# Kernel optimization log

Hardware: AMD Instinct MI355X
Metric: run time of the kernel (lower is better)

The kernel has to match this reference:

```python
import jax, jax.numpy as jnp
import numpy as np

N, C, R = 512, 32, 64   # atoms, feature channels, rbf count
EPS = 1e-8
GAMMA = 10.0
BOX = 10.0


def _eijk():
    e = np.zeros((3, 3, 3), dtype=np.float32)
    e[0, 1, 2] = e[1, 2, 0] = e[2, 0, 1] = 1.0
    e[0, 2, 1] = e[2, 1, 0] = e[1, 0, 2] = -1.0
    return jnp.asarray(e)


def setup_inputs() -> dict:
    key = jax.random.key(0)
    ks = jax.random.split(key, 8)
    d = {}
    d["geometry"] = jax.random.uniform(ks[0], (N, 3), dtype=jnp.float32) * BOX
    d["x0"] = jax.random.normal(ks[1], (N, C, 1), dtype=jnp.float32)
    d["x1"] = jax.random.normal(ks[2], (N, C, 3), dtype=jnp.float32)
    s1 = (6.0 / (R + R)) ** 0.5   # xavier_uniform for [R,R]
    s2 = (6.0 / (R + C)) ** 0.5   # xavier_uniform for [C,R]
    for i, name in enumerate(["f0", "fa", "fb", "fc"]):
        k1, k2 = jax.random.split(ks[3 + i])
        d[name + "_w1"] = jax.random.uniform(k1, (R, R), minval=-s1, maxval=s1, dtype=jnp.float32)
        d[name + "_b1"] = jnp.zeros((R,), jnp.float32)
        d[name + "_w2"] = jax.random.uniform(k2, (C, R), minval=-s2, maxval=s2, dtype=jnp.float32)
        d[name + "_b2"] = jnp.zeros((C,), jnp.float32)
    return d


def reference(geometry, x0, x1,
              f0_w1, f0_b1, f0_w2, f0_b2,
              fa_w1, fa_b1, fa_w2, fa_b2,
              fb_w1, fb_b1, fb_w2, fb_b2,
              fc_w1, fc_b1, fc_w2, fc_b2):
    # pairwise geometry: rij [N,N,3], squared dist r2 [N,N]
    rij = geometry[:, None, :] - geometry[None, :, :]
    r2 = jnp.sum(rij * rij, axis=-1)
    dij = jnp.sqrt(jnp.maximum(r2, EPS))                 # norm_with_epsilon
    centers = jnp.linspace(0.0, BOX, R, dtype=jnp.float32)
    rbf = jnp.exp(-GAMMA * (dij[..., None] - centers) ** 2)   # [N,N,R]

    self_mask = r2 < (EPS * EPS)                          # dij < EPS on true norm
    unit = rij / jnp.sqrt(r2 + EPS)[..., None]            # unit_vectors

    def radial(w1, b1, w2, b2):
        h = jax.nn.relu(jnp.einsum('abr,hr->abh', rbf, w1) + b1)
        return jnp.einsum('abh,ch->abc', h, w2) + b2      # [N,N,C]

    def f1(w1, b1, w2, b2):
        rad = jnp.where(self_mask[..., None], 0.0, radial(w1, b1, w2, b2))
        return unit[:, :, None, :] * rad[:, :, :, None]   # [N,N,C,3]

    # Filter_0 (shared radial weights) on l=0 and l=1 inputs: scalar filter, sum over neighbors b
    r0 = radial(f0_w1, f0_b1, f0_w2, f0_b2)               # [N,N,C]
    out0_a = jnp.einsum('abf,bfi->afi', r0, x0)           # [N,C,1] -> bucket 0
    out1_b = jnp.einsum('abf,bfi->afi', r0, x1)           # [N,C,3] -> bucket 1

    # filter_1_output_1 on l=0 input (cg = eye(3).unsqueeze(-1))
    F1a = f1(fa_w1, fa_b1, fa_w2, fa_b2)
    out1_a = jnp.einsum('abfi,bf->afi', F1a, x0[:, :, 0])  # [N,C,3]

    # filter_1_output_0 on l=1 input (cg = eye(3).unsqueeze(0))
    F1b = f1(fb_w1, fb_b1, fb_w2, fb_b2)
    out0_b = jnp.einsum('abfj,bfj->af', F1b, x1)[..., None]  # [N,C,1]

    # filter_1_output_1 on l=1 input (cg = eijk, cross-product coupling)
    F1c = f1(fc_w1, fc_b1, fc_w2, fc_b2)
    out1_c = jnp.einsum('ijk,abfj,bfk->afi', _eijk(), F1c, x1)  # [N,C,3]

    # concatenation() cats each bucket along channel axis (dim=-2)
    out0 = jnp.concatenate([out0_a, out0_b], axis=-2)      # [N,2C,1]
    out1 = jnp.concatenate([out1_a, out1_b, out1_c], axis=-2)  # [N,3C,3]
    return out0, out1
```

## Files before the change

### kernel.cpp

```cpp
#include <hip/hip_runtime.h>
#include <math.h>

namespace {

constexpr int NATOM = 512;
constexpr float STEP = 10.0f / 63.0f;

typedef float f32x4 __attribute__((ext_vector_type(4)));
typedef short s16x8 __attribute__((ext_vector_type(8)));

struct Ptrs { const float* p[19]; };


__device__ __forceinline__ unsigned f2bf(float f) {
  union { float f; unsigned u; } v; v.f = f;
  return (v.u + 0x7fffu + ((v.u >> 16) & 1u)) >> 16;
}

__global__ __launch_bounds__(512)
void tfn_fused(Ptrs A, float* __restrict__ out) {
  const int a    = blockIdx.x;
  const int tid  = threadIdx.x;
  const int wv   = tid >> 6;
  const int w    = wv & 3;
  const int mh   = wv >> 2;
  const int lane = tid & 63;
  const int ln   = lane & 15;
  const int hi   = lane >> 4;

  __shared__ __align__(16) short rbf_frag[2][2][2][64][8];
  __shared__ __align__(16) float u_lds[2][32][4];
  __shared__ __align__(16) short h_s[4 * 32 * 72];
  __shared__ __align__(16) float x0_s[2][32][36];
  __shared__ __align__(16) float x1_s[2][32][100];
  __shared__ __align__(16) float scr[4][16][8];

  const float* __restrict__ geom = A.p[0];
  const float* __restrict__ x0g  = A.p[1];
  const float* __restrict__ x1g  = A.p[2];

  s16x8 w1f[4][2];
  {
    const float* w1p = A.p[3 + 4 * w];
    #pragma unroll
    for (int nt = 0; nt < 4; ++nt)
      #pragma unroll
      for (int kt = 0; kt < 2; ++kt) {
        const float* src = w1p + (nt * 16 + ln) * 64 + kt * 32 + hi * 8;
        s16x8 f;
        #pragma unroll
        for (int i = 0; i < 8; ++i) f[i] = (short)f2bf(src[i]);
        w1f[nt][kt] = f;
      }
  }
  float b1v[4];
  {
    const float* b1p = A.p[4 + 4 * w];
    #pragma unroll
    for (int nt = 0; nt < 4; ++nt) b1v[nt] = b1p[nt * 16 + ln];
  }
  s16x8 w2f[2][2];
  {
    const float* w2p = A.p[5 + 4 * w];
    #pragma unroll
    for (int nt = 0; nt < 2; ++nt)
      #pragma unroll
      for (int kt = 0; kt < 2; ++kt) {
        const float* src = w2p + (nt * 16 + ln) * 64 + kt * 32 + hi * 8;
        s16x8 f;
        #pragma unroll
        for (int i = 0; i < 8; ++i) f[i] = (short)f2bf(src[i]);
        w2f[nt][kt] = f;
      }
  }
  float b2v[2];
  {
    const float* b2p = A.p[6 + 4 * w];
    b2v[0] = b2p[ln]; b2v[1] = b2p[16 + ln];
  }

  const float gax = geom[3*a+0], gay = geom[3*a+1], gaz = geom[3*a+2];

  const int sb = tid >> 4;
  const int sc = tid & 15;

  float av[8] = {0.f,0.f,0.f,0.f,0.f,0.f,0.f,0.f};

  for (int t = 0; t < 16; ++t) {
    const int b0  = t * 32;
    const int buf = t & 1;

    {
      #pragma unroll
      for (int s = 0; s < 2; ++s)
        x0_s[buf][sb][sc + 16 * s] = x0g[(b0 + sb) * 32 + sc + 16 * s];
      #pragma unroll
      for (int s = 0; s < 6; ++s)
        x1_s[buf][sb][sc + 16 * s] = x1g[(b0 + sb) * 96 + sc + 16 * s];

      const int bb = tid & 31;
      const int kq = tid >> 5;
      const int bg = b0 + bb;
      const float dx = gax - geom[3*bg+0];
      const float dy = gay - geom[3*bg+1];
      const float dz = gaz - geom[3*bg+2];
      const float r2 = dx*dx + dy*dy + dz*dz;
      const float dij = sqrtf(fmaxf(r2, 1e-8f));
      const float d0 = dij - STEP * (float)(4 * kq);
      const float d1 = d0 - STEP, d2 = d0 - 2.f*STEP, d3 = d0 - 3.f*STEP;
      const unsigned lo  = f2bf(__expf(-10.f*d0*d0)) | (f2bf(__expf(-10.f*d1*d1)) << 16);
      const unsigned hi2 = f2bf(__expf(-10.f*d2*d2)) | (f2bf(__expf(-10.f*d3*d3)) << 16);
      uint2 pk; pk.x = lo; pk.y = hi2;
      *(uint2*)&rbf_frag[buf][kq >> 3][bb >> 4][((kq >> 1) & 3) * 16 + (bb & 15)][(kq & 1) * 4] = pk;
      if (kq == 0) {
        const float inv = 1.0f / sqrtf(r2 + 1e-8f);
        f32x4 uv; uv[0] = dx*inv; uv[1] = dy*inv; uv[2] = dz*inv; uv[3] = 0.f;
        *(f32x4*)&u_lds[buf][bb][0] = uv;
      }
    }
    __syncthreads();

    const s16x8 af0 = *(const s16x8*)&rbf_frag[buf][0][mh][lane][0];
    const s16x8 af1 = *(const s16x8*)&rbf_frag[buf][1][mh][lane][0];
    f32x4 acc1[4] = {};
    #pragma unroll
    for (int nt = 0; nt < 4; ++nt)
      acc1[nt] = __builtin_amdgcn_mfma_f32_16x16x32_bf16(af0, w1f[nt][0], acc1[nt], 0, 0, 0);
    #pragma unroll
    for (int nt = 0; nt < 4; ++nt)
      acc1[nt] = __builtin_amdgcn_mfma_f32_16x16x32_bf16(af1, w1f[nt][1], acc1[nt], 0, 0, 0);
    #pragma unroll
    for (int nt = 0; nt < 4; ++nt) {
      const int j = nt * 16 + ln;
      #pragma unroll
      for (int r = 0; r < 4; ++r) {
        const int bl = mh * 16 + hi * 4 + r;
        h_s[(w * 32 + bl) * 72 + (((j >> 3) ^ (bl & 7)) << 3) + (j & 7)] =
            (short)f2bf(fmaxf(acc1[nt][r] + b1v[nt], 0.0f));
      }
    }

    const int hbase = (w * 32 + mh * 16 + ln) * 72;
    const s16x8 a20 = *(const s16x8*)&h_s[hbase + (((0 + hi) ^ (ln & 7)) << 3)];
    const s16x8 a21 = *(const s16x8*)&h_s[hbase + (((4 + hi) ^ (ln & 7)) << 3)];
    f32x4 acc2[2] = {};
    acc2[0] = __builtin_amdgcn_mfma_f32_16x16x32_bf16(a20, w2f[0][0], acc2[0], 0, 0, 0);
    acc2[1] = __builtin_amdgcn_mfma_f32_16x16x32_bf16(a20, w2f[1][0], acc2[1], 0, 0, 0);
    acc2[0] = __builtin_amdgcn_mfma_f32_16x16x32_bf16(a21, w2f[0][1], acc2[0], 0, 0, 0);
    acc2[1] = __builtin_amdgcn_mfma_f32_16x16x32_bf16(a21, w2f[1][1], acc2[1], 0, 0, 0);
    float rad0[4], rad1[4];
    #pragma unroll
    for (int e = 0; e < 4; ++e) { rad0[e] = acc2[0][e] + b2v[0]; rad1[e] = acc2[1][e] + b2v[1]; }

    const int bl4 = mh * 16 + hi * 4;
    if (w == 0) {
      #pragma unroll
      for (int e = 0; e < 4; ++e) {
        const int b = bl4 + e;
        const float r = rad0[e], s = rad1[e];
        av[0] = fmaf(r, x0_s[buf][b][ln],          av[0]);
        av[1] = fmaf(r, x1_s[buf][b][3*ln+0],      av[1]);
        av[2] = fmaf(r, x1_s[buf][b][3*ln+1],      av[2]);
        av[3] = fmaf(r, x1_s[buf][b][3*ln+2],      av[3]);
        av[4] = fmaf(s, x0_s[buf][b][16+ln],       av[4]);
        av[5] = fmaf(s, x1_s[buf][b][48+3*ln+0],   av[5]);
        av[6] = fmaf(s, x1_s[buf][b][48+3*ln+1],   av[6]);
        av[7] = fmaf(s, x1_s[buf][b][48+3*ln+2],   av[7]);
        __builtin_amdgcn_sched_barrier(0);
      }
    } else if (w == 1) {
      #pragma unroll
      for (int e = 0; e < 4; ++e) {
        const int b = bl4 + e;
        const f32x4 uv = *(const f32x4*)&u_lds[buf][b][0];
        const float rx0 = rad0[e] * x0_s[buf][b][ln];
        av[0] = fmaf(rx0, uv[0], av[0]);
        av[1] = fmaf(rx0, uv[1], av[1]);
        av[2] = fmaf(rx0, uv[2], av[2]);
        const float rx1 = rad1[e] * x0_s[buf][b][16+ln];
        av[3] = fmaf(rx1, uv[0], av[3]);
        av[4] = fmaf(rx1, uv[1], av[4]);
        av[5] = fmaf(rx1, uv[2], av[5]);
        __builtin_amdgcn_sched_barrier(0);
      }
    } else if (w == 2) {
      #pragma unroll
      for (int e = 0; e < 4; ++e) {
        const int b = bl4 + e;
        const f32x4 uv = *(const f32x4*)&u_lds[buf][b][0];
        const float dot0 = fmaf(uv[0], x1_s[buf][b][3*ln+0],
                           fmaf(uv[1], x1_s[buf][b][3*ln+1],
                                uv[2] * x1_s[buf][b][3*ln+2]));
        av[0] = fmaf(rad0[e], dot0, av[0]);
        const float dot1 = fmaf(uv[0], x1_s[buf][b][48+3*ln+0],
                           fmaf(uv[1], x1_s[buf][b][48+3*ln+1],
                                uv[2] * x1_s[buf][b][48+3*ln+2]));
        av[1] = fmaf(rad1[e], dot1, av[1]);
        __builtin_amdgcn_sched_barrier(0);
      }
    } else {
      #pragma unroll
      for (int e = 0; e < 4; ++e) {
        const int b = bl4 + e;
        const f32x4 uv = *(const f32x4*)&u_lds[buf][b][0];
        {
          const float xa = x1_s[buf][b][3*ln+0];
          const float xb = x1_s[buf][b][3*ln+1];
          const float xc = x1_s[buf][b][3*ln+2];
          const float r  = rad0[e];
          av[0] = fmaf(r, fmaf(uv[1], xc, -(uv[2] * xb)), av[0]);
          av[1] = fmaf(r, fmaf(uv[2], xa, -(uv[0] * xc)), av[1]);
          av[2] = fmaf(r, fmaf(uv[0], xb, -(uv[1] * xa)), av[2]);
        }
        {
          const float xa = x1_s[buf][b][48+3*ln+0];
          const float xb = x1_s[buf][b][48+3*ln+1];
          const float xc = x1_s[buf][b][48+3*ln+2];
          const float r  = rad1[e];
          av[3] = fmaf(r, fmaf(uv[1], xc, -(uv[2] * xb)), av[3]);
          av[4] = fmaf(r, fmaf(uv[2], xa, -(uv[0] * xc)), av[4]);
          av[5] = fmaf(r, fmaf(uv[0], xb, -(uv[1] * xa)), av[5]);
        }
        __builtin_amdgcn_sched_barrier(0);
      }
    }
  }

  #pragma unroll
  for (int q = 0; q < 8; ++q) {
    av[q] += __shfl_xor(av[q], 16);
    av[q] += __shfl_xor(av[q], 32);
  }
  if (mh == 1 && hi == 0) {
    #pragma unroll
    for (int q = 0; q < 8; ++q) scr[w][ln][q] = av[q];
  }
  __syncthreads();
  if (mh == 0 && hi == 0) {
    #pragma unroll
    for (int q = 0; q < 8; ++q) av[q] += scr[w][ln][q];
    float* o1 = out + NATOM * 64 + a * 288;
    if (w == 0) {
      out[a * 64 + ln]      = av[0];
      o1[(32 + ln) * 3 + 0] = av[1]; o1[(32 + ln) * 3 + 1] = av[2]; o1[(32 + ln) * 3 + 2] = av[3];
      out[a * 64 + 16 + ln] = av[4];
      o1[(48 + ln) * 3 + 0] = av[5]; o1[(48 + ln) * 3 + 1] = av[6]; o1[(48 + ln) * 3 + 2] = av[7];
    } else if (w == 1) {
      o1[(     ln) * 3 + 0] = av[0]; o1[(     ln) * 3 + 1] = av[1]; o1[(     ln) * 3 + 2] = av[2];
      o1[(16 + ln) * 3 + 0] = av[3]; o1[(16 + ln) * 3 + 1] = av[4]; o1[(16 + ln) * 3 + 2] = av[5];
    } else if (w == 2) {
      out[a * 64 + 32 + ln] = av[0];
      out[a * 64 + 48 + ln] = av[1];
    } else {
      o1[(64 + ln) * 3 + 0] = av[0]; o1[(64 + ln) * 3 + 1] = av[1]; o1[(64 + ln) * 3 + 2] = av[2];
      o1[(80 + ln) * 3 + 0] = av[3]; o1[(80 + ln) * 3 + 1] = av[4]; o1[(80 + ln) * 3 + 2] = av[5];
    }
  }
}

}

extern "C" void kernel_launch(void* const* d_in, const int* in_sizes, int n_in,
                              void* d_out, int out_size, void* d_ws, size_t ws_size,
                              hipStream_t stream) {
  (void)in_sizes; (void)n_in; (void)d_ws; (void)ws_size; (void)out_size;
  Ptrs A;
  for (int i = 0; i < 19; ++i) A.p[i] = (const float*)d_in[i];
  tfn_fused<<<dim3(NATOM), dim3(512), 0, stream>>>(A, (float*)d_out);
}
```

Before: 146.1 us.

## Interleave x0/x1 into one LDS array and recompute unit vectors per wave

Packs x0 and the three x1 components per channel into a single float4-aligned LDS array, so the epilogue reads two 128-bit vectors per neighbor instead of many scalar LDS loads. The unit-vector LDS buffer is dropped: waves 1-3 reload neighbor geometry from global memory and recompute the displacement and inverse norm in registers. The sched_barriers in the epilogue are removed so the compiler can reorder freely. The trade is fewer LDS loads and less LDS space against extra global geometry loads and recomputed rsqrt work per wave, plus strided global reads of x1 during staging.

```diff
diff --git a/kernel.cpp b/kernel.cpp
--- a/kernel.cpp
+++ b/kernel.cpp
@@ -29,10 +29,8 @@
   const int hi   = lane >> 4;
 
   __shared__ __align__(16) short rbf_frag[2][2][2][64][8];
-  __shared__ __align__(16) float u_lds[2][32][4];
   __shared__ __align__(16) short h_s[4 * 32 * 72];
-  __shared__ __align__(16) float x0_s[2][32][36];
-  __shared__ __align__(16) float x1_s[2][32][100];
+  __shared__ __align__(16) float xall[2][32][132];
   __shared__ __align__(16) float scr[4][16][8];
 
   const float* __restrict__ geom = A.p[0];
@@ -83,6 +81,7 @@
 
   const int sb = tid >> 4;
   const int sc = tid & 15;
+  const int bl4 = mh * 16 + hi * 4;
 
   float av[8] = {0.f,0.f,0.f,0.f,0.f,0.f,0.f,0.f};
 
@@ -90,13 +89,25 @@
     const int b0  = t * 32;
     const int buf = t & 1;
 
+    float gxe[4], gye[4], gze[4];
+    if (w != 0) {
+      const float* gp = geom + 3 * (b0 + bl4);
+      #pragma unroll
+      for (int e = 0; e < 4; ++e) {
+        gxe[e] = gp[3*e+0]; gye[e] = gp[3*e+1]; gze[e] = gp[3*e+2];
+      }
+    }
+
     {
-      #pragma unroll
-      for (int s = 0; s < 2; ++s)
-        x0_s[buf][sb][sc + 16 * s] = x0g[(b0 + sb) * 32 + sc + 16 * s];
-      #pragma unroll
-      for (int s = 0; s < 6; ++s)
-        x1_s[buf][sb][sc + 16 * s] = x1g[(b0 + sb) * 96 + sc + 16 * s];
+      const float* x0row = x0g + (b0 + sb) * 32;
+      const float* x1row = x1g + (b0 + sb) * 96;
+      f32x4 v0, v1;
+      v0[0] = x0row[sc];
+      v0[1] = x1row[3*sc+0]; v0[2] = x1row[3*sc+1]; v0[3] = x1row[3*sc+2];
+      v1[0] = x0row[sc+16];
+      v1[1] = x1row[3*(sc+16)+0]; v1[2] = x1row[3*(sc+16)+1]; v1[3] = x1row[3*(sc+16)+2];
+      *(f32x4*)&xall[buf][sb][4*sc]        = v0;
+      *(f32x4*)&xall[buf][sb][4*(sc+16)]   = v1;
 
       const int bb = tid & 31;
       const int kq = tid >> 5;
@@ -112,11 +123,6 @@
       const unsigned hi2 = f2bf(__expf(-10.f*d2*d2)) | (f2bf(__expf(-10.f*d3*d3)) << 16);
       uint2 pk; pk.x = lo; pk.y = hi2;
       *(uint2*)&rbf_frag[buf][kq >> 3][bb >> 4][((kq >> 1) & 3) * 16 + (bb & 15)][(kq & 1) * 4] = pk;
-      if (kq == 0) {
-        const float inv = 1.0f / sqrtf(r2 + 1e-8f);
-        f32x4 uv; uv[0] = dx*inv; uv[1] = dy*inv; uv[2] = dz*inv; uv[3] = 0.f;
-        *(f32x4*)&u_lds[buf][bb][0] = uv;
-      }
     }
     __syncthreads();
 
@@ -152,76 +158,50 @@
     #pragma unroll
     for (int e = 0; e < 4; ++e) { rad0[e] = acc2[0][e] + b2v[0]; rad1[e] = acc2[1][e] + b2v[1]; }
 
-    const int bl4 = mh * 16 + hi * 4;
     if (w == 0) {
       #pragma unroll
       for (int e = 0; e < 4; ++e) {
         const int b = bl4 + e;
+        const f32x4 xv0 = *(const f32x4*)&xall[buf][b][4*ln];
+        const f32x4 xv1 = *(const f32x4*)&xall[buf][b][4*(16+ln)];
         const float r = rad0[e], s = rad1[e];
-        av[0] = fmaf(r, x0_s[buf][b][ln],          av[0]);
-        av[1] = fmaf(r, x1_s[buf][b][3*ln+0],      av[1]);
-        av[2] = fmaf(r, x1_s[buf][b][3*ln+1],      av[2]);
-        av[3] = fmaf(r, x1_s[buf][b][3*ln+2],      av[3]);
-        av[4] = fmaf(s, x0_s[buf][b][16+ln],       av[4]);
-        av[5] = fmaf(s, x1_s[buf][b][48+3*ln+0],   av[5]);
-        av[6] = fmaf(s, x1_s[buf][b][48+3*ln+1],   av[6]);
-        av[7] = fmaf(s, x1_s[buf][b][48+3*ln+2],   av[7]);
-        __builtin_amdgcn_sched_barrier(0);
-      }
-    } else if (w == 1) {
+        av[0] = fmaf(r, xv0[0], av[0]);
+        av[1] = fmaf(r, xv0[1], av[1]);
+        av[2] = fmaf(r, xv0[2], av[2]);
+        av[3] = fmaf(r, xv0[3], av[3]);
+        av[4] = fmaf(s, xv1[0], av[4]);
+        av[5] = fmaf(s, xv1[1], av[5]);
+        av[6] = fmaf(s, xv1[2], av[6]);
+        av[7] = fmaf(s, xv1[3], av[7]);
+      }
+    } else {
       #pragma unroll
       for (int e = 0; e < 4; ++e) {
         const int b = bl4 + e;
-        const f32x4 uv = *(const f32x4*)&u_lds[buf][b][0];
-        const float rx0 = rad0[e] * x0_s[buf][b][ln];
-        av[0] = fmaf(rx0, uv[0], av[0]);
-        av[1] = fmaf(rx0, uv[1], av[1]);
-        av[2] = fmaf(rx0, uv[2], av[2]);
-        const float rx1 = rad1[e] * x0_s[buf][b][16+ln];
-        av[3] = fmaf(rx1, uv[0], av[3]);
-        av[4] = fmaf(rx1, uv[1], av[4]);
-        av[5] = fmaf(rx1, uv[2], av[5]);
-        __builtin_amdgcn_sched_barrier(0);
-      }
-    } else if (w == 2) {
-      #pragma unroll
-      for (int e = 0; e < 4; ++e) {
-        const int b = bl4 + e;
-        const f32x4 uv = *(const f32x4*)&u_lds[buf][b][0];
-        const float dot0 = fmaf(uv[0], x1_s[buf][b][3*ln+0],
-                           fmaf(uv[1], x1_s[buf][b][3*ln+1],
-                                uv[2] * x1_s[buf][b][3*ln+2]));
-        av[0] = fmaf(rad0[e], dot0, av[0]);
-        const float dot1 = fmaf(uv[0], x1_s[buf][b][48+3*ln+0],
-                           fmaf(uv[1], x1_s[buf][b][48+3*ln+1],
-                                uv[2] * x1_s[buf][b][48+3*ln+2]));
-        av[1] = fmaf(rad1[e], dot1, av[1]);
-        __builtin_amdgcn_sched_barrier(0);
-      }
-    } else {
-      #pragma unroll
-      for (int e = 0; e < 4; ++e) {
-        const int b = bl4 + e;
-        const f32x4 uv = *(const f32x4*)&u_lds[buf][b][0];
-        {
-          const float xa = x1_s[buf][b][3*ln+0];
-          const float xb = x1_s[buf][b][3*ln+1];
-          const float xc = x1_s[buf][b][3*ln+2];
-          const float r  = rad0[e];
-          av[0] = fmaf(r, fmaf(uv[1], xc, -(uv[2] * xb)), av[0]);
-          av[1] = fmaf(r, fmaf(uv[2], xa, -(uv[0] * xc)), av[1]);
-          av[2] = fmaf(r, fmaf(uv[0], xb, -(uv[1] * xa)), av[2]);
+        const f32x4 xv0 = *(const f32x4*)&xall[buf][b][4*ln];
+        const f32x4 xv1 = *(const f32x4*)&xall[buf][b][4*(16+ln)];
+        const float dx = gax - gxe[e], dy = gay - gye[e], dz = gaz - gze[e];
+        const float r2 = fmaf(dx, dx, fmaf(dy, dy, dz * dz));
+        const float rs = 1.0f / sqrtf(r2 + 1e-8f);
+        if (w == 1) {
+          const float t0 = rad0[e] * xv0[0] * rs;
+          av[0] = fmaf(t0, dx, av[0]); av[1] = fmaf(t0, dy, av[1]); av[2] = fmaf(t0, dz, av[2]);
+          const float t1 = rad1[e] * xv1[0] * rs;
+          av[3] = fmaf(t1, dx, av[3]); av[4] = fmaf(t1, dy, av[4]); av[5] = fmaf(t1, dz, av[5]);
+        } else if (w == 2) {
+          const float dot0 = fmaf(dx, xv0[1], fmaf(dy, xv0[2], dz * xv0[3]));
+          av[0] = fmaf(rad0[e] * rs, dot0, av[0]);
+          const float dot1 = fmaf(dx, xv1[1], fmaf(dy, xv1[2], dz * xv1[3]));
+          av[1] = fmaf(rad1[e] * rs, dot1, av[1]);
+        } else {
+          const float q0 = rad0[e] * rs, q1 = rad1[e] * rs;
+          av[0] = fmaf(q0, fmaf(dy, xv0[3], -(dz * xv0[2])), av[0]);
+          av[1] = fmaf(q0, fmaf(dz, xv0[1], -(dx * xv0[3])), av[1]);
+          av[2] = fmaf(q0, fmaf(dx, xv0[2], -(dy * xv0[1])), av[2]);
+          av[3] = fmaf(q1, fmaf(dy, xv1[3], -(dz * xv1[2])), av[3]);
+          av[4] = fmaf(q1, fmaf(dz, xv1[1], -(dx * xv1[3])), av[4]);
+          av[5] = fmaf(q1, fmaf(dx, xv1[2], -(dy * xv1[1])), av[5]);
         }
-        {
-          const float xa = x1_s[buf][b][48+3*ln+0];
-          const float xb = x1_s[buf][b][48+3*ln+1];
-          const float xc = x1_s[buf][b][48+3*ln+2];
-          const float r  = rad1[e];
-          av[3] = fmaf(r, fmaf(uv[1], xc, -(uv[2] * xb)), av[3]);
-          av[4] = fmaf(r, fmaf(uv[2], xa, -(uv[0] * xc)), av[4]);
-          av[5] = fmaf(r, fmaf(uv[0], xb, -(uv[1] * xa)), av[5]);
-        }
-        __builtin_amdgcn_sched_barrier(0);
       }
     }
   }
```

After: 177.0 us. +21.2%, slower.

## Single-buffer LDS staging, raise occupancy hint, use HIP bf16 conversion

Applied to the files above, without the earlier changes.

Replaces the double-buffered LDS staging (rbf fragments, unit vectors, x0/x1 tiles) with single buffers and adds a barrier at the top of each loop iteration to protect reuse. The smaller LDS footprint, together with a launch_bounds minimum-blocks hint of 6, is meant to let more blocks reside per CU. The hand-written float-to-bf16 rounding is swapped for the library __float2bfloat16. The cost is an extra barrier per iteration, which removes the overlap between staging the next tile and computing the current one, and the occupancy hint may force register spills.

```diff
diff --git a/kernel.cpp b/kernel.cpp
--- a/kernel.cpp
+++ b/kernel.cpp
@@ -1,4 +1,5 @@
 #include <hip/hip_runtime.h>
+#include <hip/hip_bf16.h>
 #include <math.h>
 
 namespace {
@@ -12,12 +13,13 @@
 struct Ptrs { const float* p[19]; };
 
 
-__device__ __forceinline__ unsigned f2bf(float f) {
-  union { float f; unsigned u; } v; v.f = f;
-  return (v.u + 0x7fffu + ((v.u >> 16) & 1u)) >> 16;
-}
-
-__global__ __launch_bounds__(512)
+__device__ __forceinline__ unsigned short f2bf(float f) {
+  union { __hip_bfloat16 b; unsigned short u; } v;
+  v.b = __float2bfloat16(f);
+  return v.u;
+}
+
+__global__ __launch_bounds__(512, 6)
 void tfn_fused(Ptrs A, float* __restrict__ out) {
   const int a    = blockIdx.x;
   const int tid  = threadIdx.x;
@@ -28,11 +30,11 @@
   const int ln   = lane & 15;
   const int hi   = lane >> 4;
 
-  __shared__ __align__(16) short rbf_frag[2][2][2][64][8];
-  __shared__ __align__(16) float u_lds[2][32][4];
+  __shared__ __align__(16) short rbf_frag[2][2][64][8];
   __shared__ __align__(16) short h_s[4 * 32 * 72];
-  __shared__ __align__(16) float x0_s[2][32][36];
-  __shared__ __align__(16) float x1_s[2][32][100];
+  __shared__ __align__(16) float x0_s[32][36];
+  __shared__ __align__(16) float x1_s[32][100];
+  __shared__ __align__(16) float u_lds[32][4];
   __shared__ __align__(16) float scr[4][16][8];
 
   const float* __restrict__ geom = A.p[0];
@@ -83,20 +85,22 @@
 
   const int sb = tid >> 4;
   const int sc = tid & 15;
+  const int bl4 = mh * 16 + hi * 4;
 
   float av[8] = {0.f,0.f,0.f,0.f,0.f,0.f,0.f,0.f};
 
   for (int t = 0; t < 16; ++t) {
-    const int b0  = t * 32;
-    const int buf = t & 1;
+    const int b0 = t * 32;
+
+    __syncthreads();
 
     {
       #pragma unroll
       for (int s = 0; s < 2; ++s)
-        x0_s[buf][sb][sc + 16 * s] = x0g[(b0 + sb) * 32 + sc + 16 * s];
+        x0_s[sb][sc + 16 * s] = x0g[(b0 + sb) * 32 + sc + 16 * s];
       #pragma unroll
       for (int s = 0; s < 6; ++s)
-        x1_s[buf][sb][sc + 16 * s] = x1g[(b0 + sb) * 96 + sc + 16 * s];
+        x1_s[sb][sc + 16 * s] = x1g[(b0 + sb) * 96 + sc + 16 * s];
 
       const int bb = tid & 31;
       const int kq = tid >> 5;
@@ -108,20 +112,20 @@
       const float dij = sqrtf(fmaxf(r2, 1e-8f));
       const float d0 = dij - STEP * (float)(4 * kq);
       const float d1 = d0 - STEP, d2 = d0 - 2.f*STEP, d3 = d0 - 3.f*STEP;
-      const unsigned lo  = f2bf(__expf(-10.f*d0*d0)) | (f2bf(__expf(-10.f*d1*d1)) << 16);
-      const unsigned hi2 = f2bf(__expf(-10.f*d2*d2)) | (f2bf(__expf(-10.f*d3*d3)) << 16);
+      const unsigned lo  = (unsigned)f2bf(__expf(-10.f*d0*d0)) | ((unsigned)f2bf(__expf(-10.f*d1*d1)) << 16);
+      const unsigned hi2 = (unsigned)f2bf(__expf(-10.f*d2*d2)) | ((unsigned)f2bf(__expf(-10.f*d3*d3)) << 16);
       uint2 pk; pk.x = lo; pk.y = hi2;
-      *(uint2*)&rbf_frag[buf][kq >> 3][bb >> 4][((kq >> 1) & 3) * 16 + (bb & 15)][(kq & 1) * 4] = pk;
+      *(uint2*)&rbf_frag[kq >> 3][bb >> 4][((kq >> 1) & 3) * 16 + (bb & 15)][(kq & 1) * 4] = pk;
       if (kq == 0) {
         const float inv = 1.0f / sqrtf(r2 + 1e-8f);
         f32x4 uv; uv[0] = dx*inv; uv[1] = dy*inv; uv[2] = dz*inv; uv[3] = 0.f;
-        *(f32x4*)&u_lds[buf][bb][0] = uv;
+        *(f32x4*)&u_lds[bb][0] = uv;
       }
     }
     __syncthreads();
 
-    const s16x8 af0 = *(const s16x8*)&rbf_frag[buf][0][mh][lane][0];
-    const s16x8 af1 = *(const s16x8*)&rbf_frag[buf][1][mh][lane][0];
+    const s16x8 af0 = *(const s16x8*)&rbf_frag[0][mh][lane][0];
+    const s16x8 af1 = *(const s16x8*)&rbf_frag[1][mh][lane][0];
     f32x4 acc1[4] = {};
     #pragma unroll
     for (int nt = 0; nt < 4; ++nt)
@@ -152,32 +156,31 @@
     #pragma unroll
     for (int e = 0; e < 4; ++e) { rad0[e] = acc2[0][e] + b2v[0]; rad1[e] = acc2[1][e] + b2v[1]; }
 
-    const int bl4 = mh * 16 + hi * 4;
     if (w == 0) {
       #pragma unroll
       for (int e = 0; e < 4; ++e) {
         const int b = bl4 + e;
         const float r = rad0[e], s = rad1[e];
-        av[0] = fmaf(r, x0_s[buf][b][ln],          av[0]);
-        av[1] = fmaf(r, x1_s[buf][b][3*ln+0],      av[1]);
-        av[2] = fmaf(r, x1_s[buf][b][3*ln+1],      av[2]);
-        av[3] = fmaf(r, x1_s[buf][b][3*ln+2],      av[3]);
-        av[4] = fmaf(s, x0_s[buf][b][16+ln],       av[4]);
-        av[5] = fmaf(s, x1_s[buf][b][48+3*ln+0],   av[5]);
-        av[6] = fmaf(s, x1_s[buf][b][48+3*ln+1],   av[6]);
-        av[7] = fmaf(s, x1_s[buf][b][48+3*ln+2],   av[7]);
+        av[0] = fmaf(r, x0_s[b][ln],        av[0]);
+        av[1] = fmaf(r, x1_s[b][3*ln+0],    av[1]);
+        av[2] = fmaf(r, x1_s[b][3*ln+1],    av[2]);
+        av[3] = fmaf(r, x1_s[b][3*ln+2],    av[3]);
+        av[4] = fmaf(s, x0_s[b][16+ln],     av[4]);
+        av[5] = fmaf(s, x1_s[b][48+3*ln+0], av[5]);
+        av[6] = fmaf(s, x1_s[b][48+3*ln+1], av[6]);
+        av[7] = fmaf(s, x1_s[b][48+3*ln+2], av[7]);
         __builtin_amdgcn_sched_barrier(0);
       }
     } else if (w == 1) {
       #pragma unroll
       for (int e = 0; e < 4; ++e) {
         const int b = bl4 + e;
-        const f32x4 uv = *(const f32x4*)&u_lds[buf][b][0];
-        const float rx0 = rad0[e] * x0_s[buf][b][ln];
+        const f32x4 uv = *(const f32x4*)&u_lds[b][0];
+        const float rx0 = rad0[e] * x0_s[b][ln];
         av[0] = fmaf(rx0, uv[0], av[0]);
         av[1] = fmaf(rx0, uv[1], av[1]);
         av[2] = fmaf(rx0, uv[2], av[2]);
-        const float rx1 = rad1[e] * x0_s[buf][b][16+ln];
+        const float rx1 = rad1[e] * x0_s[b][16+ln];
         av[3] = fmaf(rx1, uv[0], av[3]);
         av[4] = fmaf(rx1, uv[1], av[4]);
         av[5] = fmaf(rx1, uv[2], av[5]);
@@ -187,14 +190,14 @@
       #pragma unroll
       for (int e = 0; e < 4; ++e) {
         const int b = bl4 + e;
-        const f32x4 uv = *(const f32x4*)&u_lds[buf][b][0];
-        const float dot0 = fmaf(uv[0], x1_s[buf][b][3*ln+0],
-                           fmaf(uv[1], x1_s[buf][b][3*ln+1],
-                                uv[2] * x1_s[buf][b][3*ln+2]));
+        const f32x4 uv = *(const f32x4*)&u_lds[b][0];
+        const float dot0 = fmaf(uv[0], x1_s[b][3*ln+0],
+                           fmaf(uv[1], x1_s[b][3*ln+1],
+                                uv[2] * x1_s[b][3*ln+2]));
         av[0] = fmaf(rad0[e], dot0, av[0]);
-        const float dot1 = fmaf(uv[0], x1_s[buf][b][48+3*ln+0],
-                           fmaf(uv[1], x1_s[buf][b][48+3*ln+1],
-                                uv[2] * x1_s[buf][b][48+3*ln+2]));
+        const float dot1 = fmaf(uv[0], x1_s[b][48+3*ln+0],
+                           fmaf(uv[1], x1_s[b][48+3*ln+1],
+                                uv[2] * x1_s[b][48+3*ln+2]));
         av[1] = fmaf(rad1[e], dot1, av[1]);
         __builtin_amdgcn_sched_barrier(0);
       }
@@ -202,20 +205,20 @@
       #pragma unroll
       for (int e = 0; e < 4; ++e) {
         const int b = bl4 + e;
-        const f32x4 uv = *(const f32x4*)&u_lds[buf][b][0];
+        const f32x4 uv = *(const f32x4*)&u_lds[b][0];
         {
-          const float xa = x1_s[buf][b][3*ln+0];
-          const float xb = x1_s[buf][b][3*ln+1];
-          const float xc = x1_s[buf][b][3*ln+2];
+          const float xa = x1_s[b][3*ln+0];
+          const float xb = x1_s[b][3*ln+1];
+          const float xc = x1_s[b][3*ln+2];
           const float r  = rad0[e];
           av[0] = fmaf(r, fmaf(uv[1], xc, -(uv[2] * xb)), av[0]);
           av[1] = fmaf(r, fmaf(uv[2], xa, -(uv[0] * xc)), av[1]);
           av[2] = fmaf(r, fmaf(uv[0], xb, -(uv[1] * xa)), av[2]);
         }
         {
-          const float xa = x1_s[buf][b][48+3*ln+0];
-          const float xb = x1_s[buf][b][48+3*ln+1];
-          const float xc = x1_s[buf][b][48+3*ln+2];
+          const float xa = x1_s[b][48+3*ln+0];
+          const float xb = x1_s[b][48+3*ln+1];
+          const float xc = x1_s[b][48+3*ln+2];
           const float r  = rad1[e];
           av[3] = fmaf(r, fmaf(uv[1], xc, -(uv[2] * xb)), av[3]);
           av[4] = fmaf(r, fmaf(uv[2], xa, -(uv[0] * xc)), av[4]);
```

Result: slower. 272.0 us (+86.2%).
